# Kernel optimization log

Hardware: AMD Instinct MI355X
Metric: run time of the kernel (lower is better)

The kernel has to match this reference:

```python
import jax, jax.numpy as jnp
import numpy as np

CONF_THRESH = 0.01
IOU_THRESH = 0.5
K = 512          # fixed pre-NMS candidate count (top-K by confidence)
MAX_WH = 4096.0  # class offset for class-aware NMS (yolov5 style)
B, N, C = 16, 25200, 85  # batch, anchors (640x640 yolov5), 5+80 classes


def xywh2xyxy(b):
    xy, wh = b[..., :2], b[..., 2:4] * 0.5
    return jnp.concatenate([xy - wh, xy + wh], axis=-1)


def box_iou(a, b):
    # a: [M,4], b: [P,4] in xyxy -> [M,P]
    lt = jnp.maximum(a[:, None, :2], b[None, :, :2])
    rb = jnp.minimum(a[:, None, 2:], b[None, :, 2:])
    inter = jnp.clip(rb - lt, 0.0).prod(-1)
    area_a = (a[:, 2] - a[:, 0]) * (a[:, 3] - a[:, 1])
    area_b = (b[:, 2] - b[:, 0]) * (b[:, 3] - b[:, 1])
    return inter / (area_a[:, None] + area_b[None, :] - inter + 1e-9)


def _score_one(pred, target):
    # pred: [N, 85] = [xywh, obj, 80 class scores]
    obj = pred[:, 4]
    cls_conf = pred[:, 5:] * obj[:, None]            # obj * class prob
    conf = cls_conf.max(-1)
    cls = jnp.argmax(cls_conf, -1)
    boxes = xywh2xyxy(pred[:, :4])
    valid = (obj > CONF_THRESH) & (conf > CONF_THRESH)
    masked = jnp.where(valid, conf, -1.0)
    scores, order = jax.lax.top_k(masked, K)          # sorted desc, fixed K
    b = boxes[order]
    c = cls[order]
    v = scores > 0.0
    # class-aware NMS via coordinate offset
    off = b + c[:, None].astype(b.dtype) * MAX_WH
    iou = box_iou(off, off)                            # [K,K]
    idxs = jnp.arange(K)

    def body(i, keep):
        sup = jnp.any((iou[i] > IOU_THRESH) & keep & (idxs < i))
        return keep.at[i].set(v[i] & ~sup)

    keep = jax.lax.fori_loop(0, K, body, jnp.zeros(K, bool))

    tmask = keep & (c == target[5].astype(jnp.int32))  # correct-class kept boxes
    iou_t = box_iou(b, target[None, :4])[:, 0]         # IoU with target box
    m = jnp.where(tmask, iou_t, -1.0)
    j = jnp.argmax(m)
    return jnp.where(jnp.any(tmask), scores[j] * iou_t[j], 0.0)


def setup_inputs() -> dict:
    key = jax.random.key(0)
    k1, k2, k3, k4 = jax.random.split(key, 4)
    xy = jax.random.uniform(k1, (B, N, 2)) * 640.0
    wh = jax.random.uniform(k2, (B, N, 2)) * 160.0 + 4.0
    obj = jax.random.uniform(k3, (B, N, 1))
    cls = jax.random.uniform(k4, (B, N, C - 5))
    x = jnp.concatenate([xy, wh, obj, cls], axis=-1)
    target = jnp.array([120.0, 150.0, 360.0, 420.0, 0.9, 17.0], dtype=jnp.float32)
    return {"x": x, "target": target}


def reference(x, target):
    return jax.vmap(lambda p: _score_one(p, target))(x)  # [B]
```

## Files before the change

### kernel.cpp

```cpp
#include <hip/hip_runtime.h>
#include <stdint.h>

#pragma clang fp contract(off)

#define BB 16
#define NN 25200
#define CCH 85
#define KTOP 512
#define NBKT 1024
#define CAP 1024

#define CLSW0 1612800
#define META0 2097152
#define SB 65536

__global__ __launch_bounds__(512) void k_conf(const float* __restrict__ x,
                                              float* __restrict__ conf,
                                              uint8_t* __restrict__ clsout) {
    __shared__ float tile[128 * CCH];
    const int blk = blockIdx.x;
    const int tid = threadIdx.x;

    const float4* src = (const float4*)x + (size_t)blk * 2720;
    float4* dst = (float4*)tile;
    for (int i = tid; i < 2720; i += 512) dst[i] = src[i];
    __syncthreads();

    const int r = tid >> 2;
    const int q = tid & 3;
    const float* row = tile + r * CCH;
    const float obj = row[4];

    float best = -1.0f;
    int bi = 0;
    const float* cp = row + 5 + q * 20;
#pragma unroll
    for (int j = 0; j < 20; ++j) {
        float p = cp[j] * obj;
        if (p > best) { best = p; bi = j; }
    }
    bi += q * 20;

    float ov = __shfl_xor(best, 1);
    int oi = __shfl_xor(bi, 1);
    if (ov > best || (ov == best && oi < bi)) { best = ov; bi = oi; }
    ov = __shfl_xor(best, 2);
    oi = __shfl_xor(bi, 2);
    if (ov > best || (ov == best && oi < bi)) { best = ov; bi = oi; }

    if (q == 0) {
        const int gr = blk * 128 + r;
        const bool valid = (obj > 0.01f) && (best > 0.01f);
        conf[gr] = valid ? best : -1.0f;
        clsout[gr] = (uint8_t)bi;
    }
}

__global__ __launch_bounds__(1024) void k_sel(const float* __restrict__ x,
                                              const uint8_t* __restrict__ clsw,
                                              const float* __restrict__ conf,
                                              char* __restrict__ meta) {
    __shared__ unsigned hist[NBKT];
    __shared__ unsigned long long cand[CAP];
    __shared__ unsigned wsum[16];
    __shared__ int sh_tstar, sh_cnt;

    const int b = blockIdx.x;
    const int tid = threadIdx.x;
    const int lane = tid & 63;
    const float4* cb4 = (const float4*)(conf + (size_t)b * NN);

    hist[tid] = 0u;
    if (tid == 0) { sh_tstar = 0; sh_cnt = 0; }
    __syncthreads();
    for (int i4 = tid; i4 < NN / 4; i4 += 1024) {
        float4 c4 = cb4[i4];
        float cs[4] = {c4.x, c4.y, c4.z, c4.w};
#pragma unroll
        for (int e = 0; e < 4; ++e) {
            float c = cs[e];
            if (c > 0.0f) {
                int bk = (int)(c * 1024.0f);
                if (bk > NBKT - 1) bk = NBKT - 1;
                atomicAdd(&hist[bk], 1u);
            }
        }
    }
    __syncthreads();

    unsigned v = hist[tid];
    unsigned s = v;
#pragma unroll
    for (int d = 1; d < 64; d <<= 1) {
        unsigned t = __shfl_down(s, d);
        if (lane + d < 64) s += t;
    }
    if (lane == 0) wsum[tid >> 6] = s;
    __syncthreads();
    unsigned off = 0;
    for (int w = (tid >> 6) + 1; w < 16; ++w) off += wsum[w];
    unsigned S = s + off;
    if (S >= KTOP && (S - v) < KTOP) sh_tstar = tid;
    __syncthreads();
    const int tstar = sh_tstar;

    for (int i4 = tid; i4 < NN / 4; i4 += 1024) {
        float4 c4 = cb4[i4];
        float cs[4] = {c4.x, c4.y, c4.z, c4.w};
#pragma unroll
        for (int e = 0; e < 4; ++e) {
            float c = cs[e];
            bool want = false;
            if (c > 0.0f) {
                int bk = (int)(c * 1024.0f);
                if (bk > NBKT - 1) bk = NBKT - 1;
                want = (bk >= tstar);
            }
            unsigned long long bal = __ballot(want);
            int base = 0;
            if (lane == 0 && bal) base = atomicAdd(&sh_cnt, __popcll(bal));
            base = __shfl(base, 0);
            if (want) {
                int pos = base + __popcll(bal & ((1ull << lane) - 1ull));
                if (pos < CAP) {
                    unsigned bits = __float_as_uint(c);
                    cand[pos] = ((unsigned long long)bits << 32) | (unsigned)(~(i4 * 4 + e));
                }
            }
        }
    }
    __syncthreads();
    const int M = min(sh_cnt, CAP);

    unsigned long long key = (tid < M) ? cand[tid] : 0ull;
    __syncthreads();
    for (int kk = 2; kk <= CAP; kk <<= 1) {
        for (int j = kk >> 1; j > 0; j >>= 1) {
            unsigned long long partner;
            if (j >= 64) {
                cand[tid] = key;
                __syncthreads();
                partner = cand[tid ^ j];
                __syncthreads();
            } else {
                partner = __shfl_xor(key, j);
            }
            bool desc = (tid & kk) == 0;
            bool lower = (tid & j) == 0;
            bool take_max = (lower == desc);
            bool pg = partner > key;
            key = (take_max == pg) ? partner : key;
        }
    }

    char* mb = meta + (size_t)b * SB;
    if (tid < KTOP) {
        float sc = __uint_as_float((unsigned)(key >> 32));
        unsigned idx = ~((unsigned)key);
        bool v2 = sc > 0.0f;
        float X1 = 0.f, Y1 = 0.f, X2 = 0.f, Y2 = 0.f;
        int cl = 0;
        if (v2) {
            const float* rw = x + ((size_t)b * NN + idx) * CCH;
            float cx = rw[0], cy = rw[1];
            float w = rw[2] * 0.5f, h = rw[3] * 0.5f;
            X1 = cx - w; Y1 = cy - h; X2 = cx + w; Y2 = cy + h;
            cl = clsw[(size_t)b * NN + idx];
        }
        float offv = (float)cl * 4096.0f;
        ((float4*)mb)[tid] = make_float4(X1 + offv, Y1 + offv, X2 + offv, Y2 + offv);
        ((float4*)(mb + 8192))[tid] = make_float4(X1, Y1, X2, Y2);
        ((float*)(mb + 16384))[tid] = sc;
        ((int*)(mb + 18432))[tid] = cl;
    }
}

__global__ __launch_bounds__(1024) void k_mask(char* __restrict__ meta) {
    __shared__ float4 sox[KTOP];
    __shared__ float sarea[KTOP];
    const int slice = blockIdx.x;
    const int b = blockIdx.y;
    const int tid = threadIdx.x;
    char* mb = meta + (size_t)b * SB;

    if (tid < KTOP) {
        float4 o = ((const float4*)mb)[tid];
        sox[tid] = o;
        sarea[tid] = (o.z - o.x) * (o.w - o.y);
    }
    __syncthreads();

    const int i = slice * 64 + (tid >> 4);
    const int w = tid & 15;
    unsigned bits = 0u;
    if ((w << 5) < i) {
        float4 bi4 = sox[i];
        float ai = sarea[i];
        const int jbase = w << 5;
        for (int jj = 0; jj < 32; ++jj) {
            int j = jbase + jj;
            float4 bj = sox[j];
            float lx = fmaxf(bi4.x, bj.x);
            float ly = fmaxf(bi4.y, bj.y);
            float rx = fminf(bi4.z, bj.z);
            float ry = fminf(bi4.w, bj.w);
            float inter = fmaxf(rx - lx, 0.0f) * fmaxf(ry - ly, 0.0f);
            float den = ai + sarea[j] - inter + 1e-9f;
            float iou = inter / den;
            unsigned hit = (unsigned)((j < i) & (iou > 0.5f));
            bits |= hit << jj;
        }
    }
    ((unsigned*)(mb + 20480))[slice * 1024 + tid] = bits;
}

__global__ __launch_bounds__(1024) void k_nms(const float* __restrict__ target,
                                              const char* __restrict__ meta,
                                              float* __restrict__ out) {
    __shared__ unsigned smask[KTOP][16];
    __shared__ float4 sbb[KTOP];
    __shared__ float sscore[KTOP];
    __shared__ int scls[KTOP];
    __shared__ unsigned keep_words[16];
    __shared__ unsigned long long wred[16];

    const int b = blockIdx.x;
    const int tid = threadIdx.x;
    const char* mb = meta + (size_t)b * SB;

    const uint4* mg = (const uint4*)(mb + 20480);
    for (int p = tid; p < 2048; p += 1024) ((uint4*)smask)[p] = mg[p];
    if (tid < KTOP) {
        sbb[tid] = ((const float4*)(mb + 8192))[tid];
        sscore[tid] = ((const float*)(mb + 16384))[tid];
        scls[tid] = ((const int*)(mb + 18432))[tid];
    }
    __syncthreads();

    if (tid < 64) {
        const int l15 = tid & 15;
        unsigned keepw = 0u;
        unsigned r0 = smask[0][l15], r1 = smask[1][l15];
        float s0 = sscore[0], s1 = sscore[1];
        for (int i = 0; i < KTOP; ++i) {
            unsigned r2 = 0u; float s2 = 0.f;
            if (i < KTOP - 2) { r2 = smask[i + 2][l15]; s2 = sscore[i + 2]; }
            unsigned long long bal = __ballot((r0 & keepw) != 0u);
            bool sup = (bal & 0xFFFFull) != 0ull;
            bool kept = (s0 > 0.0f) && !sup;
            if (kept && tid == (i >> 5)) keepw |= (1u << (i & 31));
            r0 = r1; r1 = r2; s0 = s1; s1 = s2;
        }
        if (tid < 16) keep_words[tid] = keepw;
    }
    __syncthreads();

    const float tb0 = target[0], tb1 = target[1], tb2 = target[2], tb3 = target[3];
    const int tcls = (int)target[5];
    float m = -1.0f;
    if (tid < KTOP) {
        bool kept = (keep_words[tid >> 5] >> (tid & 31)) & 1u;
        if (kept && scls[tid] == tcls) {
            float4 bx = sbb[tid];
            float lx = fmaxf(bx.x, tb0);
            float ly = fmaxf(bx.y, tb1);
            float rx = fminf(bx.z, tb2);
            float ry = fminf(bx.w, tb3);
            float inter = fmaxf(rx - lx, 0.0f) * fmaxf(ry - ly, 0.0f);
            float areab = (bx.z - bx.x) * (bx.w - bx.y);
            float areat = (tb2 - tb0) * (tb3 - tb1);
            float den = areab + areat - inter + 1e-9f;
            m = inter / den;
        }
    }
    unsigned mbb = __float_as_uint(m);
    unsigned mono = (mbb & 0x80000000u) ? ~mbb : (mbb | 0x80000000u);
    unsigned long long rk = ((unsigned long long)mono << 32) | (unsigned)(~tid);
    for (int d = 32; d > 0; d >>= 1) {
        unsigned long long o = __shfl_xor(rk, d);
        if (o > rk) rk = o;
    }
    if ((tid & 63) == 0) wred[tid >> 6] = rk;
    __syncthreads();
    if (tid == 0) {
        unsigned long long bestk = wred[0];
        for (int i = 1; i < 16; ++i)
            if (wred[i] > bestk) bestk = wred[i];
        unsigned mono2 = (unsigned)(bestk >> 32);
        unsigned mbits = (mono2 & 0x80000000u) ? (mono2 & 0x7FFFFFFFu) : ~mono2;
        float mstar = __uint_as_float(mbits);
        int j = (int)(~((unsigned)bestk));
        out[b] = (mstar >= 0.0f) ? sscore[j] * mstar : 0.0f;
    }
}

extern "C" void kernel_launch(void* const* d_in, const int* in_sizes, int n_in,
                              void* d_out, int out_size, void* d_ws, size_t ws_size,
                              hipStream_t stream) {
    const float* x = (const float*)d_in[0];
    const float* target = (const float*)d_in[1];
    float* out = (float*)d_out;

    char* ws = (char*)d_ws;
    float* conf = (float*)ws;
    uint8_t* clsw = (uint8_t*)(ws + CLSW0);
    char* meta = ws + META0;

    k_conf<<<dim3((BB * NN) / 128), dim3(512), 0, stream>>>(x, conf, clsw);
    k_sel<<<dim3(BB), dim3(1024), 0, stream>>>(x, clsw, conf, meta);
    k_mask<<<dim3(8, BB), dim3(1024), 0, stream>>>(meta);
    k_nms<<<dim3(BB), dim3(1024), 0, stream>>>(target, meta, out);
}
```

Baseline: 264.9 us.

## Defer argmax class computation to top-K candidates and shrink conf blocks

Result: slower. 275.6 us (+4.0%).

```diff
diff --git a/kernel.cpp b/kernel.cpp
--- a/kernel.cpp
+++ b/kernel.cpp
@@ -10,20 +10,18 @@
 #define NBKT 1024
 #define CAP 1024
 
-#define CLSW0 1612800
 #define META0 2097152
 #define SB 65536
 
-__global__ __launch_bounds__(512) void k_conf(const float* __restrict__ x,
-                                              float* __restrict__ conf,
-                                              uint8_t* __restrict__ clsout) {
-    __shared__ float tile[128 * CCH];
+__global__ __launch_bounds__(256) void k_conf(const float* __restrict__ x,
+                                              float* __restrict__ conf) {
+    __shared__ float tile[64 * CCH];
     const int blk = blockIdx.x;
     const int tid = threadIdx.x;
 
-    const float4* src = (const float4*)x + (size_t)blk * 2720;
+    const float4* src = (const float4*)x + (size_t)blk * 1360;
     float4* dst = (float4*)tile;
-    for (int i = tid; i < 2720; i += 512) dst[i] = src[i];
+    for (int i = tid; i < 1360; i += 256) dst[i] = src[i];
     __syncthreads();
 
     const int r = tid >> 2;
@@ -32,32 +30,19 @@
     const float obj = row[4];
 
     float best = -1.0f;
-    int bi = 0;
     const float* cp = row + 5 + q * 20;
 #pragma unroll
-    for (int j = 0; j < 20; ++j) {
-        float p = cp[j] * obj;
-        if (p > best) { best = p; bi = j; }
-    }
-    bi += q * 20;
-
-    float ov = __shfl_xor(best, 1);
-    int oi = __shfl_xor(bi, 1);
-    if (ov > best || (ov == best && oi < bi)) { best = ov; bi = oi; }
-    ov = __shfl_xor(best, 2);
-    oi = __shfl_xor(bi, 2);
-    if (ov > best || (ov == best && oi < bi)) { best = ov; bi = oi; }
+    for (int j = 0; j < 20; ++j) best = fmaxf(best, cp[j] * obj);
+    best = fmaxf(best, __shfl_xor(best, 1));
+    best = fmaxf(best, __shfl_xor(best, 2));
 
     if (q == 0) {
-        const int gr = blk * 128 + r;
-        const bool valid = (obj > 0.01f) && (best > 0.01f);
-        conf[gr] = valid ? best : -1.0f;
-        clsout[gr] = (uint8_t)bi;
+        const int gr = blk * 64 + r;
+        conf[gr] = ((obj > 0.01f) && (best > 0.01f)) ? best : -1.0f;
     }
 }
 
 __global__ __launch_bounds__(1024) void k_sel(const float* __restrict__ x,
-                                              const uint8_t* __restrict__ clsw,
                                               const float* __restrict__ conf,
                                               char* __restrict__ meta) {
     __shared__ unsigned hist[NBKT];
@@ -152,26 +137,46 @@
             key = (take_max == pg) ? partner : key;
         }
     }
+    cand[tid] = key;
+    __syncthreads();
 
     char* mb = meta + (size_t)b * SB;
-    if (tid < KTOP) {
-        float sc = __uint_as_float((unsigned)(key >> 32));
-        unsigned idx = ~((unsigned)key);
-        bool v2 = sc > 0.0f;
-        float X1 = 0.f, Y1 = 0.f, X2 = 0.f, Y2 = 0.f;
-        int cl = 0;
-        if (v2) {
-            const float* rw = x + ((size_t)b * NN + idx) * CCH;
+    const int rank = tid >> 1;
+    const int half = tid & 1;
+    unsigned long long rkey = cand[rank];
+    float sc = __uint_as_float((unsigned)(rkey >> 32));
+    unsigned idx = ~((unsigned)rkey);
+    const bool v2 = sc > 0.0f;
+    float X1 = 0.f, Y1 = 0.f, X2 = 0.f, Y2 = 0.f;
+    int cl = 0;
+    if (v2) {
+        const float* rw = x + ((size_t)b * NN + idx) * CCH;
+        const float obj = rw[4];
+        float bbest = -1.0f;
+        int bi = 0;
+        const float* cp = rw + 5 + half * 40;
+#pragma unroll 8
+        for (int j = 0; j < 40; ++j) {
+            float p = cp[j] * obj;
+            if (p > bbest) { bbest = p; bi = j; }
+        }
+        bi += half * 40;
+        float ov = __shfl_xor(bbest, 1);
+        int oi = __shfl_xor(bi, 1);
+        if (half == 0) {
+            if (ov > bbest) { bbest = ov; bi = oi; }
+            cl = bi;
             float cx = rw[0], cy = rw[1];
             float w = rw[2] * 0.5f, h = rw[3] * 0.5f;
             X1 = cx - w; Y1 = cy - h; X2 = cx + w; Y2 = cy + h;
-            cl = clsw[(size_t)b * NN + idx];
-        }
+        }
+    }
+    if (half == 0) {
         float offv = (float)cl * 4096.0f;
-        ((float4*)mb)[tid] = make_float4(X1 + offv, Y1 + offv, X2 + offv, Y2 + offv);
-        ((float4*)(mb + 8192))[tid] = make_float4(X1, Y1, X2, Y2);
-        ((float*)(mb + 16384))[tid] = sc;
-        ((int*)(mb + 18432))[tid] = cl;
+        ((float4*)mb)[rank] = make_float4(X1 + offv, Y1 + offv, X2 + offv, Y2 + offv);
+        ((float4*)(mb + 8192))[rank] = make_float4(X1, Y1, X2, Y2);
+        ((float*)(mb + 16384))[rank] = sc;
+        ((int*)(mb + 18432))[rank] = cl;
     }
 }
 
@@ -197,7 +202,8 @@
         float4 bi4 = sox[i];
         float ai = sarea[i];
         const int jbase = w << 5;
-        for (int jj = 0; jj < 32; ++jj) {
+        for (int t = 0; t < 32; ++t) {
+            int jj = (t + w) & 31;
             int j = jbase + jj;
             float4 bj = sox[j];
             float lx = fmaxf(bi4.x, bj.x);
@@ -303,11 +309,10 @@
 
     char* ws = (char*)d_ws;
     float* conf = (float*)ws;
-    uint8_t* clsw = (uint8_t*)(ws + CLSW0);
     char* meta = ws + META0;
 
-    k_conf<<<dim3((BB * NN) / 128), dim3(512), 0, stream>>>(x, conf, clsw);
-    k_sel<<<dim3(BB), dim3(1024), 0, stream>>>(x, clsw, conf, meta);
+    k_conf<<<dim3((BB * NN) / 64), dim3(256), 0, stream>>>(x, conf);
+    k_sel<<<dim3(BB), dim3(1024), 0, stream>>>(x, conf, meta);
     k_mask<<<dim3(8, BB), dim3(1024), 0, stream>>>(meta);
     k_nms<<<dim3(BB), dim3(1024), 0, stream>>>(target, meta, out);
 }
```

## Build histogram in conf kernel and fold IoU mask kernel into NMS

Applied to the files above, without the earlier changes.

Result: slower. 375.0 us (+41.6%).

```diff
diff --git a/kernel.cpp b/kernel.cpp
--- a/kernel.cpp
+++ b/kernel.cpp
@@ -11,12 +11,14 @@
 #define CAP 1024
 
 #define CLSW0 1612800
+#define HIST0 2016000
 #define META0 2097152
-#define SB 65536
+#define SB 16384
 
 __global__ __launch_bounds__(512) void k_conf(const float* __restrict__ x,
                                               float* __restrict__ conf,
-                                              uint8_t* __restrict__ clsout) {
+                                              uint8_t* __restrict__ clsout,
+                                              unsigned* __restrict__ hist) {
     __shared__ float tile[128 * CCH];
     const int blk = blockIdx.x;
     const int tid = threadIdx.x;
@@ -53,14 +55,20 @@
         const bool valid = (obj > 0.01f) && (best > 0.01f);
         conf[gr] = valid ? best : -1.0f;
         clsout[gr] = (uint8_t)bi;
+        if (valid) {
+            const int b = gr / NN;
+            int bk = (int)(best * 1024.0f);
+            if (bk > NBKT - 1) bk = NBKT - 1;
+            atomicAdd(&hist[b * NBKT + bk], 1u);
+        }
     }
 }
 
 __global__ __launch_bounds__(1024) void k_sel(const float* __restrict__ x,
                                               const uint8_t* __restrict__ clsw,
                                               const float* __restrict__ conf,
+                                              const unsigned* __restrict__ hist,
                                               char* __restrict__ meta) {
-    __shared__ unsigned hist[NBKT];
     __shared__ unsigned long long cand[CAP];
     __shared__ unsigned wsum[16];
     __shared__ int sh_tstar, sh_cnt;
@@ -70,25 +78,8 @@
     const int lane = tid & 63;
     const float4* cb4 = (const float4*)(conf + (size_t)b * NN);
 
-    hist[tid] = 0u;
+    unsigned v = hist[b * NBKT + tid];
     if (tid == 0) { sh_tstar = 0; sh_cnt = 0; }
-    __syncthreads();
-    for (int i4 = tid; i4 < NN / 4; i4 += 1024) {
-        float4 c4 = cb4[i4];
-        float cs[4] = {c4.x, c4.y, c4.z, c4.w};
-#pragma unroll
-        for (int e = 0; e < 4; ++e) {
-            float c = cs[e];
-            if (c > 0.0f) {
-                int bk = (int)(c * 1024.0f);
-                if (bk > NBKT - 1) bk = NBKT - 1;
-                atomicAdd(&hist[bk], 1u);
-            }
-        }
-    }
-    __syncthreads();
-
-    unsigned v = hist[tid];
     unsigned s = v;
 #pragma unroll
     for (int d = 1; d < 64; d <<= 1) {
@@ -104,8 +95,10 @@
     __syncthreads();
     const int tstar = sh_tstar;
 
-    for (int i4 = tid; i4 < NN / 4; i4 += 1024) {
-        float4 c4 = cb4[i4];
+    for (int k = 0; k < 7; ++k) {
+        const int i4 = tid + k * 1024;
+        float4 c4 = make_float4(-1.f, -1.f, -1.f, -1.f);
+        if (i4 < NN / 4) c4 = cb4[i4];
         float cs[4] = {c4.x, c4.y, c4.z, c4.w};
 #pragma unroll
         for (int e = 0; e < 4; ++e) {
@@ -167,51 +160,10 @@
             X1 = cx - w; Y1 = cy - h; X2 = cx + w; Y2 = cy + h;
             cl = clsw[(size_t)b * NN + idx];
         }
-        float offv = (float)cl * 4096.0f;
-        ((float4*)mb)[tid] = make_float4(X1 + offv, Y1 + offv, X2 + offv, Y2 + offv);
-        ((float4*)(mb + 8192))[tid] = make_float4(X1, Y1, X2, Y2);
-        ((float*)(mb + 16384))[tid] = sc;
-        ((int*)(mb + 18432))[tid] = cl;
-    }
-}
-
-__global__ __launch_bounds__(1024) void k_mask(char* __restrict__ meta) {
-    __shared__ float4 sox[KTOP];
-    __shared__ float sarea[KTOP];
-    const int slice = blockIdx.x;
-    const int b = blockIdx.y;
-    const int tid = threadIdx.x;
-    char* mb = meta + (size_t)b * SB;
-
-    if (tid < KTOP) {
-        float4 o = ((const float4*)mb)[tid];
-        sox[tid] = o;
-        sarea[tid] = (o.z - o.x) * (o.w - o.y);
-    }
-    __syncthreads();
-
-    const int i = slice * 64 + (tid >> 4);
-    const int w = tid & 15;
-    unsigned bits = 0u;
-    if ((w << 5) < i) {
-        float4 bi4 = sox[i];
-        float ai = sarea[i];
-        const int jbase = w << 5;
-        for (int jj = 0; jj < 32; ++jj) {
-            int j = jbase + jj;
-            float4 bj = sox[j];
-            float lx = fmaxf(bi4.x, bj.x);
-            float ly = fmaxf(bi4.y, bj.y);
-            float rx = fminf(bi4.z, bj.z);
-            float ry = fminf(bi4.w, bj.w);
-            float inter = fmaxf(rx - lx, 0.0f) * fmaxf(ry - ly, 0.0f);
-            float den = ai + sarea[j] - inter + 1e-9f;
-            float iou = inter / den;
-            unsigned hit = (unsigned)((j < i) & (iou > 0.5f));
-            bits |= hit << jj;
-        }
-    }
-    ((unsigned*)(mb + 20480))[slice * 1024 + tid] = bits;
+        ((float4*)mb)[tid] = make_float4(X1, Y1, X2, Y2);
+        ((float*)(mb + 8192))[tid] = sc;
+        ((int*)(mb + 10240))[tid] = cl;
+    }
 }
 
 __global__ __launch_bounds__(1024) void k_nms(const float* __restrict__ target,
@@ -219,6 +171,8 @@
                                               float* __restrict__ out) {
     __shared__ unsigned smask[KTOP][16];
     __shared__ float4 sbb[KTOP];
+    __shared__ float4 sox[KTOP];
+    __shared__ float sarea[KTOP];
     __shared__ float sscore[KTOP];
     __shared__ int scls[KTOP];
     __shared__ unsigned keep_words[16];
@@ -228,12 +182,44 @@
     const int tid = threadIdx.x;
     const char* mb = meta + (size_t)b * SB;
 
-    const uint4* mg = (const uint4*)(mb + 20480);
-    for (int p = tid; p < 2048; p += 1024) ((uint4*)smask)[p] = mg[p];
     if (tid < KTOP) {
-        sbb[tid] = ((const float4*)(mb + 8192))[tid];
-        sscore[tid] = ((const float*)(mb + 16384))[tid];
-        scls[tid] = ((const int*)(mb + 18432))[tid];
+        float4 bx = ((const float4*)mb)[tid];
+        float sc = ((const float*)(mb + 8192))[tid];
+        int cl = ((const int*)(mb + 10240))[tid];
+        sbb[tid] = bx;
+        sscore[tid] = sc;
+        scls[tid] = cl;
+        float offv = (float)cl * 4096.0f;
+        float4 o = make_float4(bx.x + offv, bx.y + offv, bx.z + offv, bx.w + offv);
+        sox[tid] = o;
+        sarea[tid] = (o.z - o.x) * (o.w - o.y);
+    }
+    __syncthreads();
+
+    for (int p = tid; p < KTOP * 16; p += 1024) {
+        const int i = p >> 4;
+        const int w = p & 15;
+        unsigned bits = 0u;
+        if ((w << 5) < i) {
+            float4 bi4 = sox[i];
+            float ai = sarea[i];
+            const int jbase = w << 5;
+            for (int t = 0; t < 32; ++t) {
+                int jj = (t + w) & 31;
+                int j = jbase + jj;
+                float4 bj = sox[j];
+                float lx = fmaxf(bi4.x, bj.x);
+                float ly = fmaxf(bi4.y, bj.y);
+                float rx = fminf(bi4.z, bj.z);
+                float ry = fminf(bi4.w, bj.w);
+                float inter = fmaxf(rx - lx, 0.0f) * fmaxf(ry - ly, 0.0f);
+                float den = ai + sarea[j] - inter + 1e-9f;
+                float iou = inter / den;
+                unsigned hit = (unsigned)((j < i) & (iou > 0.5f));
+                bits |= hit << jj;
+            }
+        }
+        smask[i][w] = bits;
     }
     __syncthreads();
 
@@ -304,10 +290,11 @@
     char* ws = (char*)d_ws;
     float* conf = (float*)ws;
     uint8_t* clsw = (uint8_t*)(ws + CLSW0);
+    unsigned* hist = (unsigned*)(ws + HIST0);
     char* meta = ws + META0;
 
-    k_conf<<<dim3((BB * NN) / 128), dim3(512), 0, stream>>>(x, conf, clsw);
-    k_sel<<<dim3(BB), dim3(1024), 0, stream>>>(x, clsw, conf, meta);
-    k_mask<<<dim3(8, BB), dim3(1024), 0, stream>>>(meta);
+    hipMemsetAsync(hist, 0, BB * NBKT * sizeof(unsigned), stream);
+    k_conf<<<dim3((BB * NN) / 128), dim3(512), 0, stream>>>(x, conf, clsw, hist);
+    k_sel<<<dim3(BB), dim3(1024), 0, stream>>>(x, clsw, conf, hist, meta);
     k_nms<<<dim3(BB), dim3(1024), 0, stream>>>(target, meta, out);
 }
```
